# Kernel tuning notes

Measured on AMD Instinct MI355X. Metric: run time of the kernel, lower is better.

The kernel has to match this reference:

```python
import jax, jax.numpy as jnp
import numpy as np


def setup_inputs() -> dict:
    key = jax.random.key(0)
    k1, k2 = jax.random.split(key)
    h = jax.random.normal(k1, (8, 16, 64, 512), dtype=jnp.float32)
    M = jax.random.normal(k2, (20000, 512), dtype=jnp.float32)
    return {"h": h, "M": M}


def reference(h, M):
    # h: [B, T, X, R], M: [K, R]
    B, T, X, R = h.shape
    hf = h.reshape(-1, R)                      # [N, R]
    att = jax.nn.softmax(hf @ M.T, axis=1)     # [N, K], unscaled dot-product
    out = att @ M                              # [N, R]
    return out.reshape(B, T, X, R)
```

## Files before the change

kernel.cpp:

```cpp
#include <hip/hip_runtime.h>
#include <stdint.h>

#define NQ 8192
#define NK 20000
#define RD 512
#define NT 157
#define TS0 79

typedef float f32x4 __attribute__((ext_vector_type(4)));
typedef short s16x8 __attribute__((ext_vector_type(8)));

__device__ __forceinline__ unsigned short bf16_rn(float x) {
    uint32_t u = __float_as_uint(x);
    return (unsigned short)((u + 0x7FFFu + ((u >> 16) & 1)) >> 16);
}

__device__ __forceinline__ void lds_barrier() {
    asm volatile("s_waitcnt lgkmcnt(0)\n\ts_barrier" ::: "memory");
}

__global__ void preconv_kernel(const float* __restrict__ M,
                               unsigned short* __restrict__ Mhi,
                               unsigned short* __restrict__ Mlo,
                               unsigned short* __restrict__ MT) {
    __shared__ float tilef[64 * 65];
    const int k0 = blockIdx.x * 64, r0 = blockIdx.y * 64;
    const int t = threadIdx.x;
#pragma unroll
    for (int i = 0; i < 16; i++) {
        int e = t + i * 256;
        int kr = e >> 6, cc = e & 63;
        int key = k0 + kr;
        if (key < NK) {
            float x = M[(size_t)key * RD + r0 + cc];
            uint32_t u = __float_as_uint(x);
            Mhi[(size_t)key * RD + r0 + cc] = (unsigned short)(u >> 16);
            Mlo[(size_t)key * RD + r0 + cc] = bf16_rn(x - __uint_as_float(u & 0xFFFF0000u));
            tilef[cc * 65 + kr] = x;
        }
    }
    __syncthreads();
#pragma unroll
    for (int i = 0; i < 16; i++) {
        int e = t + i * 256;
        int rr = e >> 6, kk = e & 63;
        int key = k0 + kk;
        if (key < NK) MT[(size_t)(r0 + rr) * NK + key] = bf16_rn(tilef[rr * 65 + kk]);
    }
}

#define S_STEP(ii, s_) do {                                                                        \
        const int sl_ = (s_) & 1;                                                                  \
        s16x8 kh0_ = kh[0][sl_], kl0_ = kl[0][sl_];                                                \
        s16x8 kh1_ = kh[1][sl_], kl1_ = kl[1][sl_];                                                \
        {                                                                                          \
            int g_ = (ii) * 16 + (s_) + 2;                                                         \
            size_t a0_ = kaddr(g_, 0), a1_ = kaddr(g_, 1);                                         \
            kh[0][sl_] = *(const s16x8*)(Mhi + a0_);                                               \
            kl[0][sl_] = *(const s16x8*)(Mlo + a0_);                                               \
            kh[1][sl_] = *(const s16x8*)(Mhi + a1_);                                               \
            kl[1][sl_] = *(const s16x8*)(Mlo + a1_);                                               \
        }                                                                                          \
        _Pragma("unroll")                                                                          \
        for (int st_ = 0; st_ < 2; st_++) {                                                       \
            s16x8 qh_ = *(const s16x8*)&qbuf[(st_ * 16 + (s_)) * 512 + l * 8];                     \
            s16x8 ql_ = *(const s16x8*)&qbuf[16384 + (st_ * 16 + (s_)) * 512 + l * 8];             \
            C[st_][0] = __builtin_amdgcn_mfma_f32_16x16x32_bf16(qh_, kh0_, C[st_][0], 0, 0, 0);    \
            C[st_][1] = __builtin_amdgcn_mfma_f32_16x16x32_bf16(qh_, kh1_, C[st_][1], 0, 0, 0);    \
            C[st_][0] = __builtin_amdgcn_mfma_f32_16x16x32_bf16(ql_, kh0_, C[st_][0], 0, 0, 0);    \
            C[st_][1] = __builtin_amdgcn_mfma_f32_16x16x32_bf16(ql_, kh1_, C[st_][1], 0, 0, 0);    \
            C[st_][0] = __builtin_amdgcn_mfma_f32_16x16x32_bf16(qh_, kl0_, C[st_][0], 0, 0, 0);    \
            C[st_][1] = __builtin_amdgcn_mfma_f32_16x16x32_bf16(qh_, kl1_, C[st_][1], 0, 0, 0);    \
        }                                                                                          \
    } while (0)

__global__ __launch_bounds__(256, 2) void flash15_kernel(
        const float* __restrict__ h,
        const unsigned short* __restrict__ Mhi,
        const unsigned short* __restrict__ Mlo,
        const unsigned short* __restrict__ MT,
        float* __restrict__ out,
        float* __restrict__ Opart,
        float* __restrict__ mpart,
        float* __restrict__ lpart,
        int nsplit) {
    __shared__ unsigned short qbuf[32768];
    __shared__ unsigned short pbuf[8 * 512];
    __shared__ float smaxb[4 * 2 * 16];

    const int tid = threadIdx.x;
    const int ch = tid >> 6, l = tid & 63;
    const int l15 = l & 15, q4 = l >> 4;
    const int kq = (l15 >> 3) & 1, jj = l15 & 7;

    int qb, split;
    if (nsplit == 2) {
        int xcd = blockIdx.x & 7, idx = blockIdx.x >> 3;
        split = xcd >> 2;
        qb = (xcd & 3) * 64 + idx;
    } else { split = 0; qb = blockIdx.x; }
    const int koff = (split == 0) ? 0 : TS0 * 128;
    const int ntl  = (nsplit == 2) ? ((split == 0) ? TS0 : (NT - TS0)) : NT;
    const int total_ks = ntl * 16;
    const int qbase = qb * 32;

    const size_t base_w = (size_t)(ch * 32 + l15) * RD + q4 * 8;
    auto kaddr = [&](int g, int cb) -> size_t {
        if (g >= total_ks) g = total_ks - 1;
        int t2 = g >> 4, s2 = g & 15;
        return (size_t)(koff + t2 * 128) * RD + (size_t)s2 * 32 + base_w + (size_t)cb * (16 * RD);
    };

    s16x8 kh[2][2], kl[2][2];
#pragma unroll
    for (int i = 0; i < 2; i++) {
        size_t a0 = kaddr(i, 0), a1 = kaddr(i, 1);
        kh[0][i] = *(const s16x8*)(Mhi + a0);
        kl[0][i] = *(const s16x8*)(Mlo + a0);
        kh[1][i] = *(const s16x8*)(Mhi + a1);
        kl[1][i] = *(const s16x8*)(Mlo + a1);
    }

#pragma unroll
    for (int i = 0; i < 8; i++) {
        int g = tid + i * 256;
        int row = g >> 6, s = (g >> 2) & 15, qg = g & 3;
        int strip = row >> 4, lrow = row & 15;
        const float* src = h + (size_t)(qbase + row) * RD + s * 32 + qg * 8;
        f32x4 a = *(const f32x4*)src;
        f32x4 b = *(const f32x4*)(src + 4);
        s16x8 hi8, lo8;
#pragma unroll
        for (int j = 0; j < 8; j++) {
            float x = (j < 4) ? a[j] : b[j - 4];
            uint32_t u = __float_as_uint(x);
            hi8[j] = (short)(u >> 16);
            lo8[j] = (short)bf16_rn(x - __uint_as_float(u & 0xFFFF0000u));
        }
        int off = ((strip * 16 + s) * 512 + (qg * 16 + lrow) * 8);
        *(s16x8*)&qbuf[off] = hi8;
        *(s16x8*)&qbuf[16384 + off] = lo8;
    }
    lds_barrier();

    s16x8 onesf;
#pragma unroll
    for (int j = 0; j < 8; j++) onesf[j] = (short)0x3F80;

    f32x4 O[2][8];
#pragma unroll
    for (int st = 0; st < 2; st++)
#pragma unroll
        for (int ct = 0; ct < 8; ct++) O[st][ct] = 0.f;
    f32x4 Osum[2];
    Osum[0] = 0.f; Osum[1] = 0.f;
    f32x4 m_run[2];
    m_run[0] = -3e38f; m_run[1] = -3e38f;

    for (int tile = 0; tile < ntl; tile++) {
        f32x4 C[2][2];
        C[0][0] = 0.f; C[0][1] = 0.f; C[1][0] = 0.f; C[1][1] = 0.f;
#pragma unroll
        for (int s = 0; s < 16; s++) S_STEP(tile, s);
        if (tile == ntl - 1) {
#pragma unroll
            for (int cb = 0; cb < 2; cb++) {
                int kg = koff + tile * 128 + ch * 32 + cb * 16 + l15;
                if (kg >= NK) { C[0][cb] = -3e38f; C[1][cb] = -3e38f; }
            }
        }

        const unsigned short* mtp = MT + (size_t)(ch * 128 + l15) * NK + koff + tile * 128 + q4 * 8;
        s16x8 btg[2][8];
#pragma unroll
        for (int ct = 0; ct < 8; ct++) {
            btg[0][ct] = *(const s16x8*)(mtp + (size_t)ct * 16 * NK);
            btg[1][ct] = *(const s16x8*)(mtp + (size_t)ct * 16 * NK + 32);
        }

        f32x4 mx[2];
#pragma unroll
        for (int st = 0; st < 2; st++)
#pragma unroll
            for (int v = 0; v < 4; v++) mx[st][v] = fmaxf(C[st][0][v], C[st][1][v]);
#pragma unroll
        for (int d = 1; d < 16; d <<= 1) {
#pragma unroll
            for (int st = 0; st < 2; st++)
#pragma unroll
                for (int v = 0; v < 4; v++) mx[st][v] = fmaxf(mx[st][v], __shfl_xor(mx[st][v], d, 16));
        }
        if (l15 == 0) {
            *(f32x4*)&smaxb[(ch * 2 + 0) * 16 + q4 * 4] = mx[0];
            *(f32x4*)&smaxb[(ch * 2 + 1) * 16 + q4 * 4] = mx[1];
        }
        lds_barrier();
        f32x4 mnew[2]; mnew[0] = m_run[0]; mnew[1] = m_run[1];
#pragma unroll
        for (int cc = 0; cc < 4; cc++) {
#pragma unroll
            for (int st = 0; st < 2; st++) {
                f32x4 tv = *(const f32x4*)&smaxb[(cc * 2 + st) * 16 + q4 * 4];
#pragma unroll
                for (int v = 0; v < 4; v++) mnew[st][v] = fmaxf(mnew[st][v], tv[v]);
            }
        }
        f32x4 alpha[2];
#pragma unroll
        for (int st = 0; st < 2; st++)
#pragma unroll
            for (int v = 0; v < 4; v++) {
                alpha[st][v] = __expf(m_run[st][v] - mnew[st][v]);
                m_run[st][v] = mnew[st][v];
            }
#pragma unroll
        for (int st = 0; st < 2; st++) {
#pragma unroll
            for (int cb = 0; cb < 2; cb++) {
#pragma unroll
                for (int v = 0; v < 4; v++) {
                    float p = __expf(C[st][cb][v] - mnew[st][v]);
                    pbuf[(ch * 2 + st) * 512 + ((cb * 2 + kq) * 16 + q4 * 4 + v) * 8 + jj] = bf16_rn(p);
                }
            }
        }
        lds_barrier();
#pragma unroll
        for (int st = 0; st < 2; st++) {
#pragma unroll
            for (int ct = 0; ct < 8; ct++)
#pragma unroll
                for (int v = 0; v < 4; v++) O[st][ct][v] *= alpha[st][v];
#pragma unroll
            for (int v = 0; v < 4; v++) Osum[st][v] *= alpha[st][v];
        }

#pragma unroll
        for (int sk = 0; sk < 4; sk++) {
            s16x8 pa0 = *(const s16x8*)&pbuf[((sk * 2 + 0) * 512) + l * 8];
            s16x8 pa1 = *(const s16x8*)&pbuf[((sk * 2 + 1) * 512) + l * 8];
            s16x8 b0 = btg[sk & 1][0], b1 = btg[sk & 1][1], b2 = btg[sk & 1][2], b3 = btg[sk & 1][3];
            s16x8 b4 = btg[sk & 1][4], b5 = btg[sk & 1][5], b6 = btg[sk & 1][6], b7 = btg[sk & 1][7];
            if (sk < 2) {
#pragma unroll
                for (int ct = 0; ct < 8; ct++)
                    btg[sk & 1][ct] = *(const s16x8*)(mtp + (size_t)ct * 16 * NK + (sk + 2) * 32);
            }
            O[0][0] = __builtin_amdgcn_mfma_f32_16x16x32_bf16(pa0, b0, O[0][0], 0, 0, 0);
            O[1][0] = __builtin_amdgcn_mfma_f32_16x16x32_bf16(pa1, b0, O[1][0], 0, 0, 0);
            O[0][1] = __builtin_amdgcn_mfma_f32_16x16x32_bf16(pa0, b1, O[0][1], 0, 0, 0);
            O[1][1] = __builtin_amdgcn_mfma_f32_16x16x32_bf16(pa1, b1, O[1][1], 0, 0, 0);
            O[0][2] = __builtin_amdgcn_mfma_f32_16x16x32_bf16(pa0, b2, O[0][2], 0, 0, 0);
            O[1][2] = __builtin_amdgcn_mfma_f32_16x16x32_bf16(pa1, b2, O[1][2], 0, 0, 0);
            O[0][3] = __builtin_amdgcn_mfma_f32_16x16x32_bf16(pa0, b3, O[0][3], 0, 0, 0);
            O[1][3] = __builtin_amdgcn_mfma_f32_16x16x32_bf16(pa1, b3, O[1][3], 0, 0, 0);
            O[0][4] = __builtin_amdgcn_mfma_f32_16x16x32_bf16(pa0, b4, O[0][4], 0, 0, 0);
            O[1][4] = __builtin_amdgcn_mfma_f32_16x16x32_bf16(pa1, b4, O[1][4], 0, 0, 0);
            O[0][5] = __builtin_amdgcn_mfma_f32_16x16x32_bf16(pa0, b5, O[0][5], 0, 0, 0);
            O[1][5] = __builtin_amdgcn_mfma_f32_16x16x32_bf16(pa1, b5, O[1][5], 0, 0, 0);
            O[0][6] = __builtin_amdgcn_mfma_f32_16x16x32_bf16(pa0, b6, O[0][6], 0, 0, 0);
            O[1][6] = __builtin_amdgcn_mfma_f32_16x16x32_bf16(pa1, b6, O[1][6], 0, 0, 0);
            O[0][7] = __builtin_amdgcn_mfma_f32_16x16x32_bf16(pa0, b7, O[0][7], 0, 0, 0);
            O[1][7] = __builtin_amdgcn_mfma_f32_16x16x32_bf16(pa1, b7, O[1][7], 0, 0, 0);
            Osum[0] = __builtin_amdgcn_mfma_f32_16x16x32_bf16(pa0, onesf, Osum[0], 0, 0, 0);
            Osum[1] = __builtin_amdgcn_mfma_f32_16x16x32_bf16(pa1, onesf, Osum[1], 0, 0, 0);
        }
    }

    if (nsplit == 2) {
        float* Od = Opart + (size_t)split * NQ * RD;
#pragma unroll
        for (int st = 0; st < 2; st++)
#pragma unroll
            for (int ct = 0; ct < 8; ct++)
#pragma unroll
                for (int v = 0; v < 4; v++)
                    Od[(size_t)(qbase + st * 16 + q4 * 4 + v) * RD + ch * 128 + ct * 16 + l15] =
                        O[st][ct][v];
        if (ch == 0 && l15 == 0) {
#pragma unroll
            for (int st = 0; st < 2; st++)
#pragma unroll
                for (int v = 0; v < 4; v++) {
                    mpart[split * NQ + qbase + st * 16 + q4 * 4 + v] = m_run[st][v];
                    lpart[split * NQ + qbase + st * 16 + q4 * 4 + v] = Osum[st][v];
                }
        }
    } else {
#pragma unroll
        for (int st = 0; st < 2; st++)
#pragma unroll
            for (int ct = 0; ct < 8; ct++)
#pragma unroll
                for (int v = 0; v < 4; v++)
                    out[(size_t)(qbase + st * 16 + q4 * 4 + v) * RD + ch * 128 + ct * 16 + l15] =
                        O[st][ct][v] / Osum[st][v];
    }
}

__global__ __launch_bounds__(256) void combine_kernel(const float* __restrict__ Opart,
                                                      const float* __restrict__ mpart,
                                                      const float* __restrict__ lpart,
                                                      float* __restrict__ out) {
    const int t = threadIdx.x;
    const int row = blockIdx.x * 2 + (t >> 7);
    const int d = (t & 127) * 4;
    float m0 = mpart[row], m1 = mpart[NQ + row];
    float l0 = lpart[row], l1 = lpart[NQ + row];
    float m = fmaxf(m0, m1);
    float w0 = __expf(m0 - m), w1 = __expf(m1 - m);
    float inv = 1.f / (w0 * l0 + w1 * l1);
    f32x4 o0 = *(const f32x4*)&Opart[(size_t)row * RD + d];
    f32x4 o1 = *(const f32x4*)&Opart[(size_t)NQ * RD + (size_t)row * RD + d];
    f32x4 r;
#pragma unroll
    for (int v = 0; v < 4; v++) r[v] = (o0[v] * w0 + o1[v] * w1) * inv;
    *(f32x4*)&out[(size_t)row * RD + d] = r;
}

__global__ __launch_bounds__(256) void naive_kernel(const float* __restrict__ h,
                                                    const float* __restrict__ M,
                                                    float* __restrict__ out) {
    __shared__ float hs[16 * 520];
    __shared__ float ms[8 * 520];
    __shared__ float sdot[2][128];
    __shared__ float sm[16], sl[16], sal[16], sp[16][8];
    const int t = threadIdx.x;
    const int qbase = blockIdx.x * 16;
#pragma unroll
    for (int i = 0; i < 32; i++) {
        int e = t + i * 256;
        int row = e >> 9, col = e & 511;
        hs[row * 520 + col] = h[(size_t)(qbase + row) * RD + col];
    }
    if (t < 16) { sm[t] = -3e38f; sl[t] = 0.f; }
    float Oacc[32];
#pragma unroll
    for (int i = 0; i < 32; i++) Oacc[i] = 0.f;
    const int q = t >> 4;
    const int eb = (t & 15) * 32;

    for (int k0 = 0; k0 < NK; k0 += 8) {
        __syncthreads();
#pragma unroll
        for (int i = 0; i < 16; i++) {
            int e = t + i * 256;
            if (e < 4096) {
                int kk = e >> 9, col = e & 511;
                ms[kk * 520 + col] = M[(size_t)(k0 + kk) * RD + col];
            }
        }
        __syncthreads();
        {
            int pair = t & 127, half = t >> 7;
            int qq = pair & 15, kk = pair >> 4;
            const float* hp = &hs[qq * 520 + half * 256];
            const float* mp = &ms[kk * 520 + half * 256];
            float acc = 0.f;
#pragma unroll 8
            for (int e = 0; e < 256; e++) acc += hp[e] * mp[e];
            sdot[half][pair] = acc;
        }
        __syncthreads();
        if (t < 16) {
            int qq = t;
            float s8[8];
#pragma unroll
            for (int kk = 0; kk < 8; kk++) s8[kk] = sdot[0][qq + 16 * kk] + sdot[1][qq + 16 * kk];
            float mn = sm[qq];
#pragma unroll
            for (int kk = 0; kk < 8; kk++) mn = fmaxf(mn, s8[kk]);
            float al = __expf(sm[qq] - mn);
            float addl = 0.f;
#pragma unroll
            for (int kk = 0; kk < 8; kk++) { float p = __expf(s8[kk] - mn); sp[qq][kk] = p; addl += p; }
            sm[qq] = mn; sl[qq] = sl[qq] * al + addl; sal[qq] = al;
        }
        __syncthreads();
        {
            float al = sal[q];
#pragma unroll
            for (int i = 0; i < 32; i++) Oacc[i] *= al;
#pragma unroll
            for (int kk = 0; kk < 8; kk++) {
                float p = sp[q][kk];
                const float* mp = &ms[kk * 520 + eb];
#pragma unroll
                for (int i = 0; i < 32; i++) Oacc[i] += p * mp[i];
            }
        }
    }
    __syncthreads();
    float inv = 1.f / sl[q];
#pragma unroll
    for (int i = 0; i < 32; i++) out[(size_t)(qbase + q) * RD + eb + i] = Oacc[i] * inv;
}

extern "C" void kernel_launch(void* const* d_in, const int* in_sizes, int n_in,
                              void* d_out, int out_size, void* d_ws, size_t ws_size,
                              hipStream_t stream) {
    const float* h = (const float*)d_in[0];
    const float* M = (const float*)d_in[1];
    float* out = (float*)d_out;
    const size_t seg = (size_t)NK * RD;
    const size_t base_bytes = (seg * 3ull + 8192ull) * 2ull;
    const size_t opart_bytes = 2ull * NQ * RD * 4ull;
    const size_t stat_bytes = 2ull * 2ull * NQ * 4ull;
    const size_t need_split = base_bytes + opart_bytes + stat_bytes;

    if (ws_size >= base_bytes) {
        unsigned short* Mhi = (unsigned short*)d_ws;
        unsigned short* Mlo = Mhi + seg;
        unsigned short* MT  = Mlo + seg;
        float* Opart = (float*)((char*)d_ws + base_bytes);
        float* mpart = Opart + 2ull * NQ * RD;
        float* lpart = mpart + 2ull * NQ;
        preconv_kernel<<<dim3(313, 8), 256, 0, stream>>>(M, Mhi, Mlo, MT);
        if (ws_size >= need_split) {
            flash15_kernel<<<512, 256, 0, stream>>>(h, Mhi, Mlo, MT, out, Opart, mpart, lpart, 2);
            combine_kernel<<<NQ / 2, 256, 0, stream>>>(Opart, mpart, lpart, out);
        } else {
            flash15_kernel<<<256, 256, 0, stream>>>(h, Mhi, Mlo, MT, out, Opart, mpart, lpart, 1);
        }
    } else {
        naive_kernel<<<512, 256, 0, stream>>>(h, M, out);
    }
}
```

Before: 1.519 ms.

## Double wave count per block and overlap next-tile QK with softmax and PV

```diff
diff --git a/kernel.cpp b/kernel.cpp
--- a/kernel.cpp
+++ b/kernel.cpp
@@ -51,30 +51,24 @@
 
 #define S_STEP(ii, s_) do {                                                                        \
         const int sl_ = (s_) & 1;                                                                  \
-        s16x8 kh0_ = kh[0][sl_], kl0_ = kl[0][sl_];                                                \
-        s16x8 kh1_ = kh[1][sl_], kl1_ = kl[1][sl_];                                                \
+        s16x8 kh0_ = kh[sl_], kl0_ = kl[sl_];                                                      \
         {                                                                                          \
             int g_ = (ii) * 16 + (s_) + 2;                                                         \
-            size_t a0_ = kaddr(g_, 0), a1_ = kaddr(g_, 1);                                         \
-            kh[0][sl_] = *(const s16x8*)(Mhi + a0_);                                               \
-            kl[0][sl_] = *(const s16x8*)(Mlo + a0_);                                               \
-            kh[1][sl_] = *(const s16x8*)(Mhi + a1_);                                               \
-            kl[1][sl_] = *(const s16x8*)(Mlo + a1_);                                               \
+            size_t a0_ = kaddr(g_);                                                                \
+            kh[sl_] = *(const s16x8*)(Mhi + a0_);                                                  \
+            kl[sl_] = *(const s16x8*)(Mlo + a0_);                                                  \
         }                                                                                          \
         _Pragma("unroll")                                                                          \
-        for (int st_ = 0; st_ < 2; st_++) {                                                       \
+        for (int st_ = 0; st_ < 2; st_++) {                                                        \
             s16x8 qh_ = *(const s16x8*)&qbuf[(st_ * 16 + (s_)) * 512 + l * 8];                     \
             s16x8 ql_ = *(const s16x8*)&qbuf[16384 + (st_ * 16 + (s_)) * 512 + l * 8];             \
-            C[st_][0] = __builtin_amdgcn_mfma_f32_16x16x32_bf16(qh_, kh0_, C[st_][0], 0, 0, 0);    \
-            C[st_][1] = __builtin_amdgcn_mfma_f32_16x16x32_bf16(qh_, kh1_, C[st_][1], 0, 0, 0);    \
-            C[st_][0] = __builtin_amdgcn_mfma_f32_16x16x32_bf16(ql_, kh0_, C[st_][0], 0, 0, 0);    \
-            C[st_][1] = __builtin_amdgcn_mfma_f32_16x16x32_bf16(ql_, kh1_, C[st_][1], 0, 0, 0);    \
-            C[st_][0] = __builtin_amdgcn_mfma_f32_16x16x32_bf16(qh_, kl0_, C[st_][0], 0, 0, 0);    \
-            C[st_][1] = __builtin_amdgcn_mfma_f32_16x16x32_bf16(qh_, kl1_, C[st_][1], 0, 0, 0);    \
+            Cc[st_] = __builtin_amdgcn_mfma_f32_16x16x32_bf16(qh_, kh0_, Cc[st_], 0, 0, 0);        \
+            Cc[st_] = __builtin_amdgcn_mfma_f32_16x16x32_bf16(ql_, kh0_, Cc[st_], 0, 0, 0);        \
+            Cc[st_] = __builtin_amdgcn_mfma_f32_16x16x32_bf16(qh_, kl0_, Cc[st_], 0, 0, 0);        \
         }                                                                                          \
     } while (0)
 
-__global__ __launch_bounds__(256, 2) void flash15_kernel(
+__global__ __launch_bounds__(512, 2) void flash19_kernel(
         const float* __restrict__ h,
         const unsigned short* __restrict__ Mhi,
         const unsigned short* __restrict__ Mlo,
@@ -86,7 +80,7 @@
         int nsplit) {
     __shared__ unsigned short qbuf[32768];
     __shared__ unsigned short pbuf[8 * 512];
-    __shared__ float smaxb[4 * 2 * 16];
+    __shared__ float smaxb[8 * 2 * 16];
 
     const int tid = threadIdx.x;
     const int ch = tid >> 6, l = tid & 63;
@@ -104,26 +98,24 @@
     const int total_ks = ntl * 16;
     const int qbase = qb * 32;
 
-    const size_t base_w = (size_t)(ch * 32 + l15) * RD + q4 * 8;
-    auto kaddr = [&](int g, int cb) -> size_t {
+    const size_t base_w = (size_t)(ch * 16 + l15) * RD + q4 * 8;
+    auto kaddr = [&](int g) -> size_t {
         if (g >= total_ks) g = total_ks - 1;
         int t2 = g >> 4, s2 = g & 15;
-        return (size_t)(koff + t2 * 128) * RD + (size_t)s2 * 32 + base_w + (size_t)cb * (16 * RD);
+        return (size_t)(koff + t2 * 128) * RD + (size_t)s2 * 32 + base_w;
     };
 
-    s16x8 kh[2][2], kl[2][2];
+    s16x8 kh[2], kl[2];
 #pragma unroll
     for (int i = 0; i < 2; i++) {
-        size_t a0 = kaddr(i, 0), a1 = kaddr(i, 1);
-        kh[0][i] = *(const s16x8*)(Mhi + a0);
-        kl[0][i] = *(const s16x8*)(Mlo + a0);
-        kh[1][i] = *(const s16x8*)(Mhi + a1);
-        kl[1][i] = *(const s16x8*)(Mlo + a1);
-    }
-
-#pragma unroll
-    for (int i = 0; i < 8; i++) {
-        int g = tid + i * 256;
+        size_t a0 = kaddr(i);
+        kh[i] = *(const s16x8*)(Mhi + a0);
+        kl[i] = *(const s16x8*)(Mlo + a0);
+    }
+
+#pragma unroll
+    for (int i = 0; i < 4; i++) {
+        int g = tid + i * 512;
         int row = g >> 6, s = (g >> 2) & 15, qg = g & 3;
         int strip = row >> 4, lrow = row & 15;
         const float* src = h + (size_t)(qbase + row) * RD + s * 32 + qg * 8;
@@ -147,42 +139,37 @@
 #pragma unroll
     for (int j = 0; j < 8; j++) onesf[j] = (short)0x3F80;
 
-    f32x4 O[2][8];
+    f32x4 O[2][4];
 #pragma unroll
     for (int st = 0; st < 2; st++)
 #pragma unroll
-        for (int ct = 0; ct < 8; ct++) O[st][ct] = 0.f;
+        for (int ct = 0; ct < 4; ct++) O[st][ct] = 0.f;
     f32x4 Osum[2];
     Osum[0] = 0.f; Osum[1] = 0.f;
     f32x4 m_run[2];
     m_run[0] = -3e38f; m_run[1] = -3e38f;
 
-    for (int tile = 0; tile < ntl; tile++) {
-        f32x4 C[2][2];
-        C[0][0] = 0.f; C[0][1] = 0.f; C[1][0] = 0.f; C[1][1] = 0.f;
-#pragma unroll
-        for (int s = 0; s < 16; s++) S_STEP(tile, s);
-        if (tile == ntl - 1) {
-#pragma unroll
-            for (int cb = 0; cb < 2; cb++) {
-                int kg = koff + tile * 128 + ch * 32 + cb * 16 + l15;
-                if (kg >= NK) { C[0][cb] = -3e38f; C[1][cb] = -3e38f; }
-            }
-        }
-
-        const unsigned short* mtp = MT + (size_t)(ch * 128 + l15) * NK + koff + tile * 128 + q4 * 8;
-        s16x8 btg[2][8];
-#pragma unroll
-        for (int ct = 0; ct < 8; ct++) {
-            btg[0][ct] = *(const s16x8*)(mtp + (size_t)ct * 16 * NK);
-            btg[1][ct] = *(const s16x8*)(mtp + (size_t)ct * 16 * NK + 32);
+    f32x4 Cc[2];
+    Cc[0] = 0.f; Cc[1] = 0.f;
+#pragma unroll
+    for (int s = 0; s < 16; s++) S_STEP(0, s);
+
+    for (int i = 1; i <= ntl; i++) {
+        const int prv = i - 1;
+
+        f32x4 Cp[2];
+        Cp[0] = Cc[0]; Cp[1] = Cc[1];
+        Cc[0] = 0.f;   Cc[1] = 0.f;
+        if (prv == ntl - 1) {
+            int kg = koff + prv * 128 + ch * 16 + l15;
+            if (kg >= NK) { Cp[0] = -3e38f; Cp[1] = -3e38f; }
         }
 
         f32x4 mx[2];
 #pragma unroll
         for (int st = 0; st < 2; st++)
 #pragma unroll
-            for (int v = 0; v < 4; v++) mx[st][v] = fmaxf(C[st][0][v], C[st][1][v]);
+            for (int v = 0; v < 4; v++) mx[st][v] = Cp[st][v];
 #pragma unroll
         for (int d = 1; d < 16; d <<= 1) {
 #pragma unroll
@@ -194,10 +181,15 @@
             *(f32x4*)&smaxb[(ch * 2 + 0) * 16 + q4 * 4] = mx[0];
             *(f32x4*)&smaxb[(ch * 2 + 1) * 16 + q4 * 4] = mx[1];
         }
+        if (i < ntl) {
+#pragma unroll
+            for (int s = 0; s < 5; s++) S_STEP(i, s);
+        }
         lds_barrier();
+
         f32x4 mnew[2]; mnew[0] = m_run[0]; mnew[1] = m_run[1];
 #pragma unroll
-        for (int cc = 0; cc < 4; cc++) {
+        for (int cc = 0; cc < 8; cc++) {
 #pragma unroll
             for (int st = 0; st < 2; st++) {
                 f32x4 tv = *(const f32x4*)&smaxb[(cc * 2 + st) * 16 + q4 * 4];
@@ -216,35 +208,47 @@
 #pragma unroll
         for (int st = 0; st < 2; st++) {
 #pragma unroll
-            for (int cb = 0; cb < 2; cb++) {
-#pragma unroll
-                for (int v = 0; v < 4; v++) {
-                    float p = __expf(C[st][cb][v] - mnew[st][v]);
-                    pbuf[(ch * 2 + st) * 512 + ((cb * 2 + kq) * 16 + q4 * 4 + v) * 8 + jj] = bf16_rn(p);
-                }
-            }
+            for (int v = 0; v < 4; v++) {
+                float p = __expf(Cp[st][v] - mnew[st][v]);
+                pbuf[((ch >> 1) * 2 + st) * 512 +
+                     ((((ch & 1) * 2 + kq) * 16) + q4 * 4 + v) * 8 + jj] = bf16_rn(p);
+            }
+        }
+        if (i < ntl) {
+#pragma unroll
+            for (int s = 5; s < 11; s++) S_STEP(i, s);
         }
         lds_barrier();
+
 #pragma unroll
         for (int st = 0; st < 2; st++) {
 #pragma unroll
-            for (int ct = 0; ct < 8; ct++)
+            for (int ct = 0; ct < 4; ct++)
 #pragma unroll
                 for (int v = 0; v < 4; v++) O[st][ct][v] *= alpha[st][v];
 #pragma unroll
             for (int v = 0; v < 4; v++) Osum[st][v] *= alpha[st][v];
         }
-
+        const unsigned short* mtp = MT + (size_t)(ch * 64 + l15) * NK + koff + prv * 128 + q4 * 8;
+        s16x8 bt[2][4];
+#pragma unroll
+        for (int ct = 0; ct < 4; ct++) {
+            bt[0][ct] = *(const s16x8*)(mtp + (size_t)ct * 16 * NK);
+            bt[1][ct] = *(const s16x8*)(mtp + (size_t)ct * 16 * NK + 32);
+        }
+        if (i < ntl) {
+#pragma unroll
+            for (int s = 11; s < 16; s++) S_STEP(i, s);
+        }
 #pragma unroll
         for (int sk = 0; sk < 4; sk++) {
             s16x8 pa0 = *(const s16x8*)&pbuf[((sk * 2 + 0) * 512) + l * 8];
             s16x8 pa1 = *(const s16x8*)&pbuf[((sk * 2 + 1) * 512) + l * 8];
-            s16x8 b0 = btg[sk & 1][0], b1 = btg[sk & 1][1], b2 = btg[sk & 1][2], b3 = btg[sk & 1][3];
-            s16x8 b4 = btg[sk & 1][4], b5 = btg[sk & 1][5], b6 = btg[sk & 1][6], b7 = btg[sk & 1][7];
+            s16x8 b0 = bt[sk & 1][0], b1 = bt[sk & 1][1], b2 = bt[sk & 1][2], b3 = bt[sk & 1][3];
             if (sk < 2) {
 #pragma unroll
-                for (int ct = 0; ct < 8; ct++)
-                    btg[sk & 1][ct] = *(const s16x8*)(mtp + (size_t)ct * 16 * NK + (sk + 2) * 32);
+                for (int ct = 0; ct < 4; ct++)
+                    bt[sk & 1][ct] = *(const s16x8*)(mtp + (size_t)ct * 16 * NK + (sk + 2) * 32);
             }
             O[0][0] = __builtin_amdgcn_mfma_f32_16x16x32_bf16(pa0, b0, O[0][0], 0, 0, 0);
             O[1][0] = __builtin_amdgcn_mfma_f32_16x16x32_bf16(pa1, b0, O[1][0], 0, 0, 0);
@@ -254,14 +258,6 @@
             O[1][2] = __builtin_amdgcn_mfma_f32_16x16x32_bf16(pa1, b2, O[1][2], 0, 0, 0);
             O[0][3] = __builtin_amdgcn_mfma_f32_16x16x32_bf16(pa0, b3, O[0][3], 0, 0, 0);
             O[1][3] = __builtin_amdgcn_mfma_f32_16x16x32_bf16(pa1, b3, O[1][3], 0, 0, 0);
-            O[0][4] = __builtin_amdgcn_mfma_f32_16x16x32_bf16(pa0, b4, O[0][4], 0, 0, 0);
-            O[1][4] = __builtin_amdgcn_mfma_f32_16x16x32_bf16(pa1, b4, O[1][4], 0, 0, 0);
-            O[0][5] = __builtin_amdgcn_mfma_f32_16x16x32_bf16(pa0, b5, O[0][5], 0, 0, 0);
-            O[1][5] = __builtin_amdgcn_mfma_f32_16x16x32_bf16(pa1, b5, O[1][5], 0, 0, 0);
-            O[0][6] = __builtin_amdgcn_mfma_f32_16x16x32_bf16(pa0, b6, O[0][6], 0, 0, 0);
-            O[1][6] = __builtin_amdgcn_mfma_f32_16x16x32_bf16(pa1, b6, O[1][6], 0, 0, 0);
-            O[0][7] = __builtin_amdgcn_mfma_f32_16x16x32_bf16(pa0, b7, O[0][7], 0, 0, 0);
-            O[1][7] = __builtin_amdgcn_mfma_f32_16x16x32_bf16(pa1, b7, O[1][7], 0, 0, 0);
             Osum[0] = __builtin_amdgcn_mfma_f32_16x16x32_bf16(pa0, onesf, Osum[0], 0, 0, 0);
             Osum[1] = __builtin_amdgcn_mfma_f32_16x16x32_bf16(pa1, onesf, Osum[1], 0, 0, 0);
         }
@@ -272,10 +268,10 @@
 #pragma unroll
         for (int st = 0; st < 2; st++)
 #pragma unroll
-            for (int ct = 0; ct < 8; ct++)
+            for (int ct = 0; ct < 4; ct++)
 #pragma unroll
                 for (int v = 0; v < 4; v++)
-                    Od[(size_t)(qbase + st * 16 + q4 * 4 + v) * RD + ch * 128 + ct * 16 + l15] =
+                    Od[(size_t)(qbase + st * 16 + q4 * 4 + v) * RD + ch * 64 + ct * 16 + l15] =
                         O[st][ct][v];
         if (ch == 0 && l15 == 0) {
 #pragma unroll
@@ -290,10 +286,10 @@
 #pragma unroll
         for (int st = 0; st < 2; st++)
 #pragma unroll
-            for (int ct = 0; ct < 8; ct++)
+            for (int ct = 0; ct < 4; ct++)
 #pragma unroll
                 for (int v = 0; v < 4; v++)
-                    out[(size_t)(qbase + st * 16 + q4 * 4 + v) * RD + ch * 128 + ct * 16 + l15] =
+                    out[(size_t)(qbase + st * 16 + q4 * 4 + v) * RD + ch * 64 + ct * 16 + l15] =
                         O[st][ct][v] / Osum[st][v];
     }
 }
@@ -417,10 +413,10 @@
         float* lpart = mpart + 2ull * NQ;
         preconv_kernel<<<dim3(313, 8), 256, 0, stream>>>(M, Mhi, Mlo, MT);
         if (ws_size >= need_split) {
-            flash15_kernel<<<512, 256, 0, stream>>>(h, Mhi, Mlo, MT, out, Opart, mpart, lpart, 2);
+            flash19_kernel<<<512, 512, 0, stream>>>(h, Mhi, Mlo, MT, out, Opart, mpart, lpart, 2);
             combine_kernel<<<NQ / 2, 256, 0, stream>>>(Opart, mpart, lpart, out);
         } else {
-            flash15_kernel<<<256, 256, 0, stream>>>(h, Mhi, Mlo, MT, out, Opart, mpart, lpart, 1);
+            flash19_kernel<<<256, 512, 0, stream>>>(h, Mhi, Mlo, MT, out, Opart, mpart, lpart, 1);
         }
     } else {
         naive_kernel<<<512, 256, 0, stream>>>(h, M, out);
```

After: 1.787 ms. 1.18x slower.
